# Kernel tuning notes

Measured on AMD Instinct MI355X. Metric: run time of the kernel, lower is better.

Reference implementation:

```python
import jax, jax.numpy as jnp
import numpy as np

DIM = 768
N_HEADS = 12
HEAD_DIM = DIM // N_HEADS
HIDDEN = 4 * DIM
EPS = 1e-5


def _layernorm(x, gamma, beta):
    mu = jnp.mean(x, axis=-1, keepdims=True)
    var = jnp.mean(jnp.square(x - mu), axis=-1, keepdims=True)
    return (x - mu) * jax.lax.rsqrt(var + EPS) * gamma + beta


def setup_inputs() -> dict:
    key = jax.random.key(0)
    ks = jax.random.split(key, 8)
    B, N = 16, 1024
    s = 0.02
    return {
        "x": jax.random.normal(ks[0], (B, N, DIM), jnp.float32),
        "Wqkv": jax.random.normal(ks[1], (DIM, 3 * DIM), jnp.float32) * s,
        "bqkv": jnp.zeros((3 * DIM,), jnp.float32),
        "Wproj": jax.random.normal(ks[2], (DIM, DIM), jnp.float32) * s,
        "bproj": jnp.zeros((DIM,), jnp.float32),
        "g1": jnp.ones((DIM,), jnp.float32),
        "b1": jnp.zeros((DIM,), jnp.float32),
        "g2": jnp.ones((DIM,), jnp.float32),
        "b2": jnp.zeros((DIM,), jnp.float32),
        "W1": jax.random.normal(ks[3], (DIM, HIDDEN), jnp.float32) * s,
        "bf1": jnp.zeros((HIDDEN,), jnp.float32),
        "W2": jax.random.normal(ks[4], (HIDDEN, DIM), jnp.float32) * s,
        "bf2": jnp.zeros((DIM,), jnp.float32),
    }


def reference(x, Wqkv, bqkv, Wproj, bproj, g1, b1, g2, b2, W1, bf1, W2, bf2):
    B, N, _ = x.shape
    # --- attention branch (pre-LN) ---
    h = _layernorm(x, g1, b1)
    qkv = (h @ Wqkv + bqkv).reshape(B, N, 3, N_HEADS, HEAD_DIM)
    qkv = jnp.transpose(qkv, (2, 0, 3, 1, 4))  # [3, B, H, N, D]
    q, k, v = qkv[0], qkv[1], qkv[2]
    # NOTE: source scales by dim**-0.5, not head_dim**-0.5 (faithful)
    scores = jnp.einsum("bhnd,bhmd->bhnm", q, k) * (DIM ** -0.5)
    attn = jax.nn.softmax(scores, axis=-1)
    out = jnp.einsum("bhnm,bhmd->bhnd", attn, v)
    out = jnp.transpose(out, (0, 2, 1, 3)).reshape(B, N, DIM)
    x = x + (out @ Wproj + bproj)
    # --- MLP branch ---
    h2 = _layernorm(x, g2, b2)
    ff = jax.nn.relu(h2 @ W1 + bf1) @ W2 + bf2
    return x + ff
```

## Files before the change

### kernel.cpp

```cpp
#include <hip/hip_runtime.h>
#include <cstdint>
#include <cstddef>

typedef unsigned short u16;
typedef __bf16 bf16x8 __attribute__((ext_vector_type(8)));
typedef unsigned short u16x8 __attribute__((ext_vector_type(8)));
typedef float f32x4 __attribute__((ext_vector_type(4)));

#define DIMN 768
#define BNROWS 16384
#define NH 12
#define HD 64
#define HID 3072
#define QKVN 2304

__device__ __forceinline__ u16 f2bf(float f) {
  unsigned u = __builtin_bit_cast(unsigned, f);
  u += 0x7fffu + ((u >> 16) & 1u);
  return (u16)(u >> 16);
}

__device__ __forceinline__ bf16x8 ld8(const u16* p) {
  u16x8 v = *reinterpret_cast<const u16x8*>(p);
  return __builtin_bit_cast(bf16x8, v);
}

__device__ __forceinline__ void gload16(const void* g, void* l) {
  __builtin_amdgcn_global_load_lds(
      (const __attribute__((address_space(1))) unsigned int*)g,
      (__attribute__((address_space(3))) unsigned int*)l, 16, 0, 0);
}

#define MFMA(a, b, c) __builtin_amdgcn_mfma_f32_16x16x32_bf16(a, b, c, 0, 0, 0)

__global__ __launch_bounds__(256) void twb_k(const float* __restrict__ W,
                                             u16* __restrict__ Wt, int K, int N) {
  __shared__ float tile[32][33];
  const int n0 = blockIdx.x * 32, k0 = blockIdx.y * 32;
  const int tx = threadIdx.x & 31, ty = threadIdx.x >> 5;
#pragma unroll
  for (int i = 0; i < 4; i++)
    tile[ty + i * 8][tx] = W[(size_t)(k0 + ty + i * 8) * N + n0 + tx];
  __syncthreads();
#pragma unroll
  for (int i = 0; i < 4; i++)
    Wt[(size_t)(n0 + ty + i * 8) * K + k0 + tx] = f2bf(tile[tx][ty + i * 8]);
}

__global__ __launch_bounds__(256) void ln_k(const float* __restrict__ x,
                                            const float* __restrict__ g,
                                            const float* __restrict__ bta,
                                            u16* __restrict__ outp) {
  const int row = blockIdx.x * 4 + (threadIdx.x >> 6);
  const int lane = threadIdx.x & 63;
  const float4* xr = (const float4*)(x + (size_t)row * DIMN);
  float4 v[3];
  float s = 0.f, ss = 0.f;
#pragma unroll
  for (int c = 0; c < 3; c++) {
    v[c] = xr[c * 64 + lane];
    s += v[c].x + v[c].y + v[c].z + v[c].w;
    ss += v[c].x * v[c].x + v[c].y * v[c].y + v[c].z * v[c].z + v[c].w * v[c].w;
  }
#pragma unroll
  for (int off = 1; off < 64; off <<= 1) {
    s += __shfl_xor(s, off);
    ss += __shfl_xor(ss, off);
  }
  const float mu = s * (1.f / DIMN);
  const float var = ss * (1.f / DIMN) - mu * mu;
  const float rs = rsqrtf(var + 1e-5f);
  u16* orow = outp + (size_t)row * DIMN;
#pragma unroll
  for (int c = 0; c < 3; c++) {
    float4 gv = ((const float4*)g)[c * 64 + lane];
    float4 bv = ((const float4*)bta)[c * 64 + lane];
    ushort4 o;
    o.x = f2bf((v[c].x - mu) * rs * gv.x + bv.x);
    o.y = f2bf((v[c].y - mu) * rs * gv.y + bv.y);
    o.z = f2bf((v[c].z - mu) * rs * gv.z + bv.z);
    o.w = f2bf((v[c].w - mu) * rs * gv.w + bv.w);
    ((ushort4*)orow)[c * 64 + lane] = o;
  }
}

template <int OUT_BF16, int RELU, int RESID>
__global__ __launch_bounds__(512, 2) void gemm256_k(const u16* __restrict__ A,
                                                    const u16* __restrict__ Bt,
                                                    const float* __restrict__ bias,
                                                    const float* __restrict__ resid,
                                                    void* __restrict__ Cout, int N, int K) {
  __shared__ u16 lds[65536];
  const int tid = threadIdx.x;
  const int m0 = blockIdx.x * 256;
  const int n0 = blockIdx.y * 256;
  const int lane = tid & 63, w = tid >> 6;
  const int wr = w >> 2, wc = w & 3;
  const int lhi = lane >> 4, llo = lane & 15;
  const int NT = K >> 5;

  const int srow = tid >> 2, sc8 = (tid & 3) * 8;
  const u16* aS0 = A + (size_t)(m0 + srow) * K + sc8;
  const u16* aS1 = A + (size_t)(m0 + 128 + srow) * K + sc8;
  const u16* bS0 = Bt + (size_t)(n0 + srow) * K + sc8;
  const u16* bS1 = Bt + (size_t)(n0 + 128 + srow) * K + sc8;

  auto slotBase = [&](int t) -> char* { return (char*)lds + ((size_t)(t & 3) << 15); };
  auto stageA = [&](int t) {
    char* sb = slotBase(t);
    gload16(aS0 + t * 32, sb + tid * 16);
    gload16(aS1 + t * 32, sb + 8192 + tid * 16);
  };
  auto stageB = [&](int t) {
    char* sb = slotBase(t) + 16384;
    gload16(bS0 + t * 32, sb + tid * 16);
    gload16(bS1 + t * 32, sb + 8192 + tid * 16);
  };

  f32x4 acc[8][4] = {};

  stageA(0); stageB(0);
  stageA(1); stageB(1);
  stageA(2); stageB(2);
  asm volatile("s_waitcnt vmcnt(8)" ::: "memory");
  __builtin_amdgcn_s_barrier();

  for (int t = 0; t < NT; ++t) {
    const char* sb = slotBase(t);
    bf16x8 af[4], bfr[4];
#pragma unroll
    for (int ni = 0; ni < 4; ni++)
      bfr[ni] = ld8((const u16*)(sb + 16384 + (wc * 64 + ni * 16 + llo) * 64 + lhi * 16));
#pragma unroll
    for (int mi = 0; mi < 4; mi++)
      af[mi] = ld8((const u16*)(sb + (wr * 128 + mi * 16 + llo) * 64 + lhi * 16));
    if (t + 3 < NT) stageA(t + 3);
    __builtin_amdgcn_s_barrier();
    asm volatile("s_waitcnt lgkmcnt(0)" ::: "memory");
    __builtin_amdgcn_sched_barrier(0);
    __builtin_amdgcn_s_setprio(1);
#pragma unroll
    for (int mi = 0; mi < 4; mi++)
#pragma unroll
      for (int ni = 0; ni < 4; ni++) acc[mi][ni] = MFMA(af[mi], bfr[ni], acc[mi][ni]);
    __builtin_amdgcn_s_setprio(0);
    __builtin_amdgcn_sched_barrier(0);
    __builtin_amdgcn_s_barrier();
#pragma unroll
    for (int mi = 0; mi < 4; mi++)
      af[mi] = ld8((const u16*)(sb + (wr * 128 + 64 + mi * 16 + llo) * 64 + lhi * 16));
    if (t + 3 < NT) stageB(t + 3);
    __builtin_amdgcn_s_barrier();
    asm volatile("s_waitcnt lgkmcnt(0)" ::: "memory");
    __builtin_amdgcn_sched_barrier(0);
    __builtin_amdgcn_s_setprio(1);
#pragma unroll
    for (int mi = 0; mi < 4; mi++)
#pragma unroll
      for (int ni = 0; ni < 4; ni++) acc[4 + mi][ni] = MFMA(af[mi], bfr[ni], acc[4 + mi][ni]);
    __builtin_amdgcn_s_setprio(0);
    __builtin_amdgcn_sched_barrier(0);
    if (t + 3 < NT) {
      asm volatile("s_waitcnt vmcnt(8)" ::: "memory");
    } else if (t + 2 < NT) {
      asm volatile("s_waitcnt vmcnt(4)" ::: "memory");
    } else if (t + 1 < NT) {
      asm volatile("s_waitcnt vmcnt(0)" ::: "memory");
    }
    __builtin_amdgcn_s_barrier();
  }

#pragma unroll
  for (int mi = 0; mi < 8; mi++)
#pragma unroll
    for (int ni = 0; ni < 4; ni++) {
      const int row = m0 + wr * 128 + mi * 16 + lhi * 4;
      const int col = n0 + wc * 64 + ni * 16 + llo;
      const float bsv = bias[col];
#pragma unroll
      for (int rr = 0; rr < 4; rr++) {
        float v = acc[mi][ni][rr] + bsv;
        if (RELU) v = fmaxf(v, 0.0f);
        const size_t idx = (size_t)(row + rr) * N + col;
        if (RESID) v += resid[idx];
        if (OUT_BF16)
          ((u16*)Cout)[idx] = f2bf(v);
        else
          ((float*)Cout)[idx] = v;
      }
    }
}

__device__ __forceinline__ bf16x8 ldscale8(const u16* p, float c) {
  u16x8 v = *reinterpret_cast<const u16x8*>(p);
  bf16x8 r;
#pragma unroll
  for (int j = 0; j < 8; j++) {
    float f = __builtin_bit_cast(float, (unsigned)v[j] << 16) * c;
    r[j] = (__bf16)f;
  }
  return r;
}

__device__ __forceinline__ unsigned pack_bf2(float a, float b) {
  unsigned ua = (unsigned)__builtin_bit_cast(u16, (__bf16)a);
  unsigned ub = (unsigned)__builtin_bit_cast(u16, (__bf16)b);
  return ua | (ub << 16);
}

__global__ __launch_bounds__(256) void attn_k(const u16* __restrict__ qkv,
                                              u16* __restrict__ outp) {
  __shared__ u16 Vt[64 * 64];
  __shared__ u16 Ps[4][32 * 64];

  const int tid = threadIdx.x;
  const int f = blockIdx.x;
  const int bh = (f & 7) | ((f >> 6) << 3);
  const int qt = (f >> 3) & 7;
  const int b = bh / NH, h = bh - b * NH;
  const int lane = tid & 63, w = tid >> 6;
  const int lhi = lane >> 4, llo = lane & 15;
  const size_t rowb = (size_t)b * 1024;
  const int wq0 = qt * 128 + w * 32;
  const float SC = 0.052059750f;

  bf16x8 qb[2][2];
#pragma unroll
  for (int mi = 0; mi < 2; mi++) {
    const u16* qrow = qkv + (rowb + wq0 + mi * 16 + llo) * QKVN + h * HD;
    qb[mi][0] = ldscale8(qrow + lhi * 8, SC);
    qb[mi][1] = ldscale8(qrow + 32 + lhi * 8, SC);
  }

  const u16* kbase = qkv + rowb * QKVN + DIMN + h * HD;
  const u16* vbase = qkv + rowb * QKVN + 2 * DIMN + h * HD;
  const int vc8 = w * 8;
  const int sw = (llo & 7) * 8;

  float psum[2] = {0.f, 0.f};
  f32x4 oacc[2][4] = {};

  for (int kt = 0; kt < 16; kt++) {
    u16x8 v0 = *reinterpret_cast<const u16x8*>(vbase + (kt * 64 + lane) * QKVN + vc8);
    u16x8 v1 = *reinterpret_cast<const u16x8*>(vbase + (kt * 64 + lane) * QKVN + vc8 + 32);
    bf16x8 kf[2][4];
#pragma unroll
    for (int ks = 0; ks < 2; ks++)
#pragma unroll
      for (int ni = 0; ni < 4; ni++)
        kf[ks][ni] = ld8(kbase + (kt * 64 + ni * 16 + llo) * QKVN + ks * 32 + lhi * 8);

    __syncthreads();
#pragma unroll
    for (int j = 0; j < 8; j++) {
      Vt[(vc8 + j) * 64 + (lane ^ (j * 8))] = v0[j];
      Vt[(vc8 + 32 + j) * 64 + (lane ^ (j * 8))] = v1[j];
    }
    __syncthreads();

    f32x4 sacc[4][2] = {};
#pragma unroll
    for (int ks = 0; ks < 2; ks++)
#pragma unroll
      for (int ni = 0; ni < 4; ni++)
#pragma unroll
        for (int mi = 0; mi < 2; mi++)
          sacc[ni][mi] = MFMA(kf[ks][ni], qb[mi][ks], sacc[ni][mi]);

#pragma unroll
    for (int mi = 0; mi < 2; mi++)
#pragma unroll
      for (int ni = 0; ni < 4; ni++) {
        float p0 = __builtin_amdgcn_exp2f(sacc[ni][mi][0]);
        float p1 = __builtin_amdgcn_exp2f(sacc[ni][mi][1]);
        float p2 = __builtin_amdgcn_exp2f(sacc[ni][mi][2]);
        float p3 = __builtin_amdgcn_exp2f(sacc[ni][mi][3]);
        psum[mi] += (p0 + p1) + (p2 + p3);
        u16* pp = &Ps[w][(mi * 16 + llo) * 64 + ((ni * 16 + lhi * 4) ^ sw)];
        ((unsigned*)pp)[0] = pack_bf2(p0, p1);
        ((unsigned*)pp)[1] = pack_bf2(p2, p3);
      }

#pragma unroll
    for (int ks = 0; ks < 2; ks++) {
      const int koff = ks * 32 + lhi * 8;
      bf16x8 pa0 = ld8(&Ps[w][llo * 64 + (koff ^ sw)]);
      bf16x8 pa1 = ld8(&Ps[w][(16 + llo) * 64 + (koff ^ sw)]);
#pragma unroll
      for (int ni = 0; ni < 4; ni++) {
        bf16x8 vb = ld8(&Vt[(ni * 16 + llo) * 64 + (koff ^ sw)]);
        oacc[0][ni] = MFMA(pa0, vb, oacc[0][ni]);
        oacc[1][ni] = MFMA(pa1, vb, oacc[1][ni]);
      }
    }
  }

  float rl[2][4];
#pragma unroll
  for (int mi = 0; mi < 2; mi++) {
    psum[mi] += __shfl_xor(psum[mi], 16);
    psum[mi] += __shfl_xor(psum[mi], 32);
#pragma unroll
    for (int r = 0; r < 4; r++) rl[mi][r] = 1.0f / __shfl(psum[mi], lhi * 4 + r);
  }

#pragma unroll
  for (int mi = 0; mi < 2; mi++)
#pragma unroll
    for (int ni = 0; ni < 4; ni++)
#pragma unroll
      for (int r = 0; r < 4; r++) {
        const size_t row = rowb + wq0 + mi * 16 + lhi * 4 + r;
        outp[row * DIMN + h * HD + ni * 16 + llo] = f2bf(oacc[mi][ni][r] * rl[mi][r]);
      }
}

extern "C" void kernel_launch(void* const* d_in, const int* in_sizes, int n_in,
                              void* d_out, int out_size, void* d_ws, size_t ws_size,
                              hipStream_t stream) {
  const float* x = (const float*)d_in[0];
  const float* Wqkv = (const float*)d_in[1];
  const float* bqkv = (const float*)d_in[2];
  const float* Wproj = (const float*)d_in[3];
  const float* bproj = (const float*)d_in[4];
  const float* g1 = (const float*)d_in[5];
  const float* b1 = (const float*)d_in[6];
  const float* g2 = (const float*)d_in[7];
  const float* b2 = (const float*)d_in[8];
  const float* W1 = (const float*)d_in[9];
  const float* bf1 = (const float*)d_in[10];
  const float* W2 = (const float*)d_in[11];
  const float* bf2 = (const float*)d_in[12];
  float* outp = (float*)d_out;

  char* p = (char*)d_ws;
  u16* WqkvT = (u16*)p; p += (size_t)QKVN * DIMN * 2;
  u16* WprojT = (u16*)p; p += (size_t)DIMN * DIMN * 2;
  u16* W1T = (u16*)p; p += (size_t)HID * DIMN * 2;
  u16* W2T = (u16*)p; p += (size_t)DIMN * HID * 2;
  u16* bufX = (u16*)p; p += (size_t)BNROWS * DIMN * 2;
  u16* big = (u16*)p; p += (size_t)BNROWS * HID * 2;

  twb_k<<<dim3(QKVN / 32, DIMN / 32), 256, 0, stream>>>(Wqkv, WqkvT, DIMN, QKVN);
  twb_k<<<dim3(DIMN / 32, DIMN / 32), 256, 0, stream>>>(Wproj, WprojT, DIMN, DIMN);
  twb_k<<<dim3(HID / 32, DIMN / 32), 256, 0, stream>>>(W1, W1T, DIMN, HID);
  twb_k<<<dim3(DIMN / 32, HID / 32), 256, 0, stream>>>(W2, W2T, HID, DIMN);

  ln_k<<<BNROWS / 4, 256, 0, stream>>>(x, g1, b1, bufX);
  gemm256_k<1, 0, 0><<<dim3(64, QKVN / 256), 512, 0, stream>>>(bufX, WqkvT, bqkv, nullptr,
                                                               big, QKVN, DIMN);
  attn_k<<<1536, 256, 0, stream>>>(big, bufX);
  gemm256_k<0, 0, 1><<<dim3(64, DIMN / 256), 512, 0, stream>>>(bufX, WprojT, bproj, x, outp,
                                                               DIMN, DIMN);
  ln_k<<<BNROWS / 4, 256, 0, stream>>>(outp, g2, b2, bufX);
  gemm256_k<1, 1, 0><<<dim3(64, HID / 256), 512, 0, stream>>>(bufX, W1T, bf1, nullptr, big,
                                                              HID, DIMN);
  gemm256_k<0, 0, 1><<<dim3(64, DIMN / 256), 512, 0, stream>>>(big, W2T, bf2, outp, outp,
                                                               DIMN, HID);
}
```

Baseline: 495.6 us.

## Double-buffer K and V tiles in LDS with async prefetch in attention

The attention kernel now stages K tiles into double-buffered shared memory using direct global-to-LDS loads, and prefetches the next V tile into registers while the current tile is being computed. V is also double-buffered in LDS, and synchronization moves to explicit waitcnt and barriers. The goal is to hide global load latency behind the MFMA and exp work instead of stalling at the top of each iteration. The P writes are also merged into one 64-bit store. In exchange, LDS use goes up, which may lower occupancy, and the hand-written vmcnt counts must match the order in which loads are issued.

```diff
diff --git a/kernel.cpp b/kernel.cpp
--- a/kernel.cpp
+++ b/kernel.cpp
@@ -210,7 +210,8 @@
 
 __global__ __launch_bounds__(256) void attn_k(const u16* __restrict__ qkv,
                                               u16* __restrict__ outp) {
-  __shared__ u16 Vt[64 * 64];
+  __shared__ u16 Ks[2][64 * 64];
+  __shared__ u16 Vt[2][64 * 64];
   __shared__ u16 Ps[4][32 * 64];
 
   const int tid = threadIdx.x;
@@ -236,36 +237,61 @@
   const u16* vbase = qkv + rowb * QKVN + 2 * DIMN + h * HD;
   const int vc8 = w * 8;
   const int sw = (llo & 7) * 8;
+  const int rsw = llo & 7;
+
+  const int srow = tid >> 3, su = tid & 7;
+  const u16* ksrc = kbase + (size_t)srow * QKVN + (su ^ (srow & 7)) * 8;
+
+  auto stageK = [&](int kt, int buf) {
+    const u16* s0 = ksrc + (size_t)kt * 64 * QKVN;
+    gload16(s0, (char*)&Ks[buf][0] + tid * 16);
+    gload16(s0 + (size_t)32 * QKVN, (char*)&Ks[buf][0] + 4096 + tid * 16);
+  };
+  auto loadV = [&](int kt, u16x8& a, u16x8& c) {
+    const u16* vr = vbase + (size_t)(kt * 64 + lane) * QKVN + vc8;
+    a = *reinterpret_cast<const u16x8*>(vr);
+    c = *reinterpret_cast<const u16x8*>(vr + 32);
+  };
+  auto writeV = [&](int buf, u16x8 a, u16x8 c) {
+#pragma unroll
+    for (int j = 0; j < 8; j++) {
+      Vt[buf][(vc8 + j) * 64 + (lane ^ (j * 8))] = a[j];
+      Vt[buf][(vc8 + 32 + j) * 64 + (lane ^ (j * 8))] = c[j];
+    }
+  };
+
+  u16x8 v0, v1, nv0, nv1;
+
+  stageK(0, 0);
+  loadV(0, v0, v1);
+  stageK(1, 1);
+  asm volatile("s_waitcnt vmcnt(2)" ::: "memory");
+  writeV(0, v0, v1);
+  asm volatile("s_waitcnt lgkmcnt(0)" ::: "memory");
+  __builtin_amdgcn_s_barrier();
+  __builtin_amdgcn_sched_barrier(0);
 
   float psum[2] = {0.f, 0.f};
   f32x4 oacc[2][4] = {};
 
-  for (int kt = 0; kt < 16; kt++) {
-    u16x8 v0 = *reinterpret_cast<const u16x8*>(vbase + (kt * 64 + lane) * QKVN + vc8);
-    u16x8 v1 = *reinterpret_cast<const u16x8*>(vbase + (kt * 64 + lane) * QKVN + vc8 + 32);
-    bf16x8 kf[2][4];
+  for (int t = 0; t < 16; t++) {
+    if (t < 15) loadV(t + 1, nv0, nv1);
+
+    const u16* kB = &Ks[t & 1][0];
+    f32x4 sacc[4][2] = {};
 #pragma unroll
     for (int ks = 0; ks < 2; ks++)
 #pragma unroll
-      for (int ni = 0; ni < 4; ni++)
-        kf[ks][ni] = ld8(kbase + (kt * 64 + ni * 16 + llo) * QKVN + ks * 32 + lhi * 8);
-
-    __syncthreads();
-#pragma unroll
-    for (int j = 0; j < 8; j++) {
-      Vt[(vc8 + j) * 64 + (lane ^ (j * 8))] = v0[j];
-      Vt[(vc8 + 32 + j) * 64 + (lane ^ (j * 8))] = v1[j];
-    }
-    __syncthreads();
-
-    f32x4 sacc[4][2] = {};
-#pragma unroll
-    for (int ks = 0; ks < 2; ks++)
-#pragma unroll
-      for (int ni = 0; ni < 4; ni++)
-#pragma unroll
-        for (int mi = 0; mi < 2; mi++)
-          sacc[ni][mi] = MFMA(kf[ks][ni], qb[mi][ks], sacc[ni][mi]);
+      for (int ni = 0; ni < 4; ni++) {
+        bf16x8 kf = ld8(&kB[(ni * 16 + llo) * 64 + (((ks * 4 + lhi) ^ rsw) * 8)]);
+#pragma unroll
+        for (int mi = 0; mi < 2; mi++) sacc[ni][mi] = MFMA(kf, qb[mi][ks], sacc[ni][mi]);
+      }
+
+    asm volatile("s_waitcnt lgkmcnt(0)" ::: "memory");
+    __builtin_amdgcn_s_barrier();
+    __builtin_amdgcn_sched_barrier(0);
+    if (t + 2 < 16) stageK(t + 2, t & 1);
 
 #pragma unroll
     for (int mi = 0; mi < 2; mi++)
@@ -277,8 +303,10 @@
         float p3 = __builtin_amdgcn_exp2f(sacc[ni][mi][3]);
         psum[mi] += (p0 + p1) + (p2 + p3);
         u16* pp = &Ps[w][(mi * 16 + llo) * 64 + ((ni * 16 + lhi * 4) ^ sw)];
-        ((unsigned*)pp)[0] = pack_bf2(p0, p1);
-        ((unsigned*)pp)[1] = pack_bf2(p2, p3);
+        uint2 pw;
+        pw.x = pack_bf2(p0, p1);
+        pw.y = pack_bf2(p2, p3);
+        *reinterpret_cast<uint2*>(pp) = pw;
       }
 
 #pragma unroll
@@ -288,10 +316,23 @@
       bf16x8 pa1 = ld8(&Ps[w][(16 + llo) * 64 + (koff ^ sw)]);
 #pragma unroll
       for (int ni = 0; ni < 4; ni++) {
-        bf16x8 vb = ld8(&Vt[(ni * 16 + llo) * 64 + (koff ^ sw)]);
+        bf16x8 vb = ld8(&Vt[t & 1][(ni * 16 + llo) * 64 + (koff ^ sw)]);
         oacc[0][ni] = MFMA(pa0, vb, oacc[0][ni]);
         oacc[1][ni] = MFMA(pa1, vb, oacc[1][ni]);
       }
+    }
+
+    if (t < 15) {
+      if (t + 2 < 16) {
+        asm volatile("s_waitcnt vmcnt(2)" ::: "memory");
+      } else {
+        asm volatile("s_waitcnt vmcnt(0)" ::: "memory");
+      }
+      writeV((t + 1) & 1, nv0, nv1);
+      v0 = nv0; v1 = nv1;
+      asm volatile("s_waitcnt lgkmcnt(0)" ::: "memory");
+      __builtin_amdgcn_s_barrier();
+      __builtin_amdgcn_sched_barrier(0);
     }
   }
 
```

Measured after the change: 462.4 us. 6.7% less time.
